# Performance work log

Measured on AMD Instinct MI355X. Metric: run time of the kernel, lower is better.

## Reference

```python
import jax, jax.numpy as jnp
import numpy as np

H = 512

def setup_inputs() -> dict:
    key = jax.random.key(0)
    k1, k2, k3, k4 = jax.random.split(key, 4)
    B, S_dec, S_enc = 8, 2048, 2048
    encoder_output = jax.random.normal(k1, (B, S_enc, H), dtype=jnp.float32)
    decoder_output = jax.random.normal(k2, (B, S_dec, H), dtype=jnp.float32)
    # nn.Bilinear(H, H, 1): weight [1, H, H], bias [1]; init U(-1/sqrt(H), 1/sqrt(H))
    bound = 1.0 / np.sqrt(H)
    W = jax.random.uniform(k3, (1, H, H), dtype=jnp.float32, minval=-bound, maxval=bound)
    b = jax.random.uniform(k4, (1,), dtype=jnp.float32, minval=-bound, maxval=bound)
    return {"encoder_output": encoder_output, "decoder_output": decoder_output, "W": W, "b": b}

def reference(encoder_output, decoder_output, W, b):
    # Original: scores[b,d,e] = Bilinear(enc[b,e], dec[b,d]) = enc[b,e] @ W[0] @ dec[b,d] + bias
    # Computed as two GEMMs instead of expanding to [B, S_dec, S_enc, H].
    encW = jnp.einsum('beh,hg->beg', encoder_output, W[0])   # [B, S_enc, H]
    scores = jnp.einsum('beg,bdg->bde', encW, decoder_output) + b[0]  # [B, S_dec, S_enc]
    return scores
```

## Files before the change

kernel.cpp:

```cpp
#include <hip/hip_runtime.h>

typedef __attribute__((ext_vector_type(8))) short short8;
typedef __attribute__((ext_vector_type(4))) float f32x4;
typedef __attribute__((ext_vector_type(8))) unsigned short ushort8;

__device__ __forceinline__ unsigned short f2bf(float x) {
  union { float f; unsigned u; } v; v.f = x;
  unsigned r = v.u + 0x7fffu + ((v.u >> 16) & 1u);
  return (unsigned short)(r >> 16);
}

__global__ __launch_bounds__(256) void wt_kernel(
    const float* __restrict__ W, unsigned short* __restrict__ Wt) {
  __shared__ float s[64][65];
  int g0 = blockIdx.x * 64, h0 = blockIdx.y * 64;
  int tx = threadIdx.x & 63, ty = threadIdx.x >> 6;
#pragma unroll
  for (int rr = 0; rr < 16; ++rr) {
    int h = ty * 16 + rr;
    s[h][tx] = W[(long)(h0 + h) * 512 + g0 + tx];
  }
  __syncthreads();
#pragma unroll
  for (int rr = 0; rr < 16; ++rr) {
    int g = ty * 16 + rr;
    Wt[(long)(g0 + g) * 512 + h0 + tx] = f2bf(s[tx][g]);
  }
}

__global__ __launch_bounds__(256) void gemm1_plus_cvtdec(
    const float* __restrict__ enc, const unsigned short* __restrict__ Wt,
    unsigned short* __restrict__ encW,
    const float* __restrict__ dec, unsigned short* __restrict__ dec_bf) {
  if (blockIdx.x >= 512) {
    int i = (blockIdx.x - 512) * 256 + threadIdx.x;
    const float4* p = (const float4*)(dec + (long)i * 8);
    float4 a = p[0], b = p[1];
    ushort8 o;
    o[0] = f2bf(a.x); o[1] = f2bf(a.y); o[2] = f2bf(a.z); o[3] = f2bf(a.w);
    o[4] = f2bf(b.x); o[5] = f2bf(b.y); o[6] = f2bf(b.z); o[7] = f2bf(b.w);
    *(ushort8*)(dec_bf + (long)i * 8) = o;
    return;
  }

  constexpr int K = 512, N = 512, BK = 32;
  __shared__ __align__(16) short As[128 * BK];
  __shared__ __align__(16) short Bs[128 * BK];

  const int g = blockIdx.x;
  const int work = (g & 7) * 64 + (g >> 3);
  const int bxm = work >> 2, byn = work & 3;

  const int tid = threadIdx.x;
  const int wave = tid >> 6, lane = tid & 63;
  const int wm = wave >> 1, wn = wave & 1;
  const int r = lane & 15, q = lane >> 4;

  const float* Ab = enc + (long)bxm * 128 * K;
  const unsigned short* Bb = Wt + (long)byn * 128 * K;

  const int srow = tid >> 1, shalf = tid & 1;
  const float* arow = Ab + (long)srow * K + shalf * 16;

  f32x4 acc[4][4] = {};
  float4 av[4];
#pragma unroll
  for (int j = 0; j < 4; ++j) av[j] = ((const float4*)arow)[j];

  for (int kt = 0; kt < K; kt += BK) {
    ushort8 o0, o1;
    o0[0] = f2bf(av[0].x); o0[1] = f2bf(av[0].y); o0[2] = f2bf(av[0].z); o0[3] = f2bf(av[0].w);
    o0[4] = f2bf(av[1].x); o0[5] = f2bf(av[1].y); o0[6] = f2bf(av[1].z); o0[7] = f2bf(av[1].w);
    o1[0] = f2bf(av[2].x); o1[1] = f2bf(av[2].y); o1[2] = f2bf(av[2].z); o1[3] = f2bf(av[2].w);
    o1[4] = f2bf(av[3].x); o1[5] = f2bf(av[3].y); o1[6] = f2bf(av[3].z); o1[7] = f2bf(av[3].w);
    *(ushort8*)&As[srow * BK + shalf * 16 + 0] = o0;
    *(ushort8*)&As[srow * BK + shalf * 16 + 8] = o1;

#pragma unroll
    for (int j = 0; j < 2; ++j) {
      int c = (j * 4 + wave) * 64 + lane;
      int row = c >> 2;
      int coff = (c & 3) * 8;
      __builtin_amdgcn_global_load_lds(
          (const __attribute__((address_space(1))) void*)(Bb + (long)row * K + kt + coff),
          (__attribute__((address_space(3))) void*)(Bs + (j * 4 + wave) * 512),
          16, 0, 0);
    }
    __syncthreads();

    short8 af[4], bfr[4];
#pragma unroll
    for (int m = 0; m < 4; ++m)
      af[m] = *(const short8*)&As[(wm * 64 + m * 16 + r) * BK + q * 8];
#pragma unroll
    for (int n = 0; n < 4; ++n)
      bfr[n] = *(const short8*)&Bs[(wn * 64 + n * 16 + r) * BK + q * 8];

    if (kt + BK < K) {
      const float* ap = arow + kt + BK;
#pragma unroll
      for (int j = 0; j < 4; ++j) av[j] = ((const float4*)ap)[j];
    }

#pragma unroll
    for (int m = 0; m < 4; ++m)
#pragma unroll
      for (int n = 0; n < 4; ++n)
        acc[m][n] = __builtin_amdgcn_mfma_f32_16x16x32_bf16(af[m], bfr[n], acc[m][n], 0, 0, 0);
    __syncthreads();
  }

  const long rowbase = (long)bxm * 128 + wm * 64;
  const long colbase = (long)byn * 128 + wn * 64;
#pragma unroll
  for (int m = 0; m < 4; ++m)
#pragma unroll
    for (int n = 0; n < 4; ++n)
#pragma unroll
      for (int j = 0; j < 4; ++j) {
        long row = rowbase + m * 16 + q * 4 + j;
        long col = colbase + n * 16 + r;
        encW[row * (long)N + col] = f2bf(acc[m][n][j]);
      }
}

#define VMCNT(n) asm volatile("s_waitcnt vmcnt(" #n ")" ::: "memory")
#define LGKM0  asm volatile("s_waitcnt lgkmcnt(0)" ::: "memory")
#define BAR __builtin_amdgcn_s_barrier()

#define LA(p, h) (Lds + (p) * 32768 + (h) * 16384)
#define LB(p, h) (Lds + 65536 + (p) * 32768 + (h) * 16384)

#define STGH(GP, LBASE, T, H)                                                 \
  do {                                                                        \
    _Pragma("unroll") for (int j_ = 0; j_ < 2; ++j_) {                        \
      int c_ = w * 2 + j_;                                                    \
      __builtin_amdgcn_global_load_lds(                                       \
          (const __attribute__((address_space(1))) void*)(                    \
              (GP) + ((long)((H) * 128 + (c_ >> 1) * 16 + srow)) * 512 +      \
              (T) * 64 + (c_ & 1) * 32 + scol),                               \
          (__attribute__((address_space(3))) void*)((LBASE) + (c_ << 10)),    \
          16, 0, 0);                                                          \
    }                                                                         \
  } while (0)

#define LOADAF(p, mh)                                                         \
  _Pragma("unroll") for (int mi_ = 0; mi_ < 4; ++mi_)                         \
    _Pragma("unroll") for (int ks_ = 0; ks_ < 2; ++ks_)                       \
      af[mi_][ks_] = *(const short8*)(LA(p, wm) +                             \
          ((((mh) * 4 + mi_) * 2 + ks_) << 10) + lconst)

#define LOADBF(p, nh)                                                         \
  _Pragma("unroll") for (int n_ = 0; n_ < 2; ++n_)                            \
    _Pragma("unroll") for (int ks_ = 0; ks_ < 2; ++ks_)                       \
      bf[nh][n_][ks_] = *(const short8*)(LB(p, wn >> 1) +                     \
          ((((wn & 1) * 4 + (nh) * 2 + n_) * 2 + ks_) << 10) + lconst)

#define QMFMA(mh, nh)                                                         \
  do {                                                                        \
    BAR;                                                                      \
    LGKM0;                                                                    \
    __builtin_amdgcn_sched_barrier(0);                                        \
    __builtin_amdgcn_s_setprio(1);                                            \
    _Pragma("unroll") for (int mi_ = 0; mi_ < 4; ++mi_)                       \
      _Pragma("unroll") for (int n_ = 0; n_ < 2; ++n_)                        \
        _Pragma("unroll") for (int ks_ = 0; ks_ < 2; ++ks_)                   \
          acc[(mh) * 4 + mi_][(nh) * 2 + n_] =                                \
              __builtin_amdgcn_mfma_f32_16x16x32_bf16(                        \
                  af[mi_][ks_], bf[nh][n_][ks_],                              \
                  acc[(mh) * 4 + mi_][(nh) * 2 + n_], 0, 0, 0);               \
    __builtin_amdgcn_s_setprio(0);                                            \
  } while (0)

__global__ __launch_bounds__(512) void gemm2_8ph2(
    const unsigned short* __restrict__ A,
    const unsigned short* __restrict__ Bt,
    float* __restrict__ C, const float* __restrict__ bias) {
  __shared__ __align__(16) char Lds[131072];

  const int flat = blockIdx.x;
  const int z = flat & 7;
  const int work = flat >> 3;
  const int by = work & 7, bx = work >> 3;

  const int tid = threadIdx.x;
  const int w = tid >> 6, lane = tid & 63;
  const int wm = w >> 2, wn = w & 3;
  const int base_r = lane & 15, q = lane >> 4;
  const int lconst = base_r * 64 + ((q * 16) ^ ((base_r & 8) << 2));
  const int srow = lane >> 2;
  const int scol = ((lane & 3) * 8) ^ (((lane >> 5) & 1) << 4);

  const unsigned short* Ab = A + ((long)z * 2048 + bx * 256) * 512;
  const unsigned short* Bb = Bt + ((long)z * 2048 + by * 256) * 512;

  f32x4 acc[8][4] = {};
  short8 af[4][2];
  short8 bf[2][2][2];

  STGH(Bb, LB(0, 0), 0, 0);
  STGH(Bb, LB(0, 1), 0, 1);
  STGH(Ab, LA(0, 0), 0, 0);
  STGH(Ab, LA(0, 1), 0, 1);
  STGH(Bb, LB(1, 0), 1, 0);
  STGH(Ab, LA(1, 0), 1, 0);
  VMCNT(4);
  BAR;

  for (int t = 0; t < 3; ++t) {
    const int T1v = 2 * t + 1, T2v = 2 * t + 2, T3v = 2 * t + 3;
    LOADAF(0, 0); LOADBF(0, 0);
    STGH(Ab, LA(1, 1), T1v, 1);
    QMFMA(0, 0); BAR;
    LOADBF(0, 1);
    STGH(Bb, LB(1, 1), T1v, 1);
    QMFMA(0, 1); BAR;
    LOADAF(0, 1);
    STGH(Bb, LB(0, 0), T2v, 0);
    QMFMA(1, 0); BAR;
    STGH(Bb, LB(0, 1), T2v, 1);
    QMFMA(1, 1); VMCNT(4); BAR;
    LOADAF(1, 0); LOADBF(1, 0);
    STGH(Ab, LA(0, 0), T2v, 0);
    QMFMA(0, 0); BAR;
    LOADBF(1, 1);
    STGH(Ab, LA(0, 1), T2v, 1);
    QMFMA(0, 1); BAR;
    LOADAF(1, 1);
    STGH(Bb, LB(1, 0), T3v, 0);
    QMFMA(1, 0); BAR;
    STGH(Ab, LA(1, 0), T3v, 0);
    QMFMA(1, 1); VMCNT(4); BAR;
  }
  LOADAF(0, 0); LOADBF(0, 0);
  STGH(Ab, LA(1, 1), 7, 1);
  QMFMA(0, 0); BAR;
  LOADBF(0, 1);
  STGH(Bb, LB(1, 1), 7, 1);
  QMFMA(0, 1); BAR;
  LOADAF(0, 1);               QMFMA(1, 0); BAR;
                              QMFMA(1, 1); VMCNT(0); BAR;
  LOADAF(1, 0); LOADBF(1, 0); QMFMA(0, 0); BAR;
  LOADBF(1, 1);               QMFMA(0, 1); BAR;
  LOADAF(1, 1);               QMFMA(1, 0); BAR;
                              QMFMA(1, 1);

  const float bv = bias[0];
  float* Cb = C + ((long)z * 2048 + bx * 256 + wm * 128) * 2048 + by * 256 + wn * 64;
#pragma unroll
  for (int m = 0; m < 8; ++m)
#pragma unroll
    for (int n = 0; n < 4; ++n)
#pragma unroll
      for (int j = 0; j < 4; ++j)
        Cb[(long)(m * 16 + q * 4 + j) * 2048 + n * 16 + base_r] = acc[m][n][j] + bv;
}

extern "C" void kernel_launch(void* const* d_in, const int* in_sizes, int n_in,
                              void* d_out, int out_size, void* d_ws, size_t ws_size,
                              hipStream_t stream) {
  const float* enc  = (const float*)d_in[0];
  const float* dec  = (const float*)d_in[1];
  const float* W    = (const float*)d_in[2];
  const float* bias = (const float*)d_in[3];
  float* out = (float*)d_out;

  constexpr int Bn = 8, S = 2048, H = 512;
  constexpr long NE = (long)Bn * S * H;

  unsigned short* dec_bf = (unsigned short*)d_ws;
  unsigned short* Wt     = dec_bf + NE;
  unsigned short* encW   = Wt + (long)H * H;

  wt_kernel<<<dim3(8, 8), 256, 0, stream>>>(W, Wt);

  gemm1_plus_cvtdec<<<dim3(512 + 4096, 1, 1), 256, 0, stream>>>(
      enc, Wt, encW, dec, dec_bf);

  gemm2_8ph2<<<dim3(512, 1, 1), 512, 0, stream>>>(dec_bf, encW, out, bias);
}
```

Baseline: 79.57 us.

## Compute two adjacent output tiles per block in second GEMM, reusing A tile

Each block of the second GEMM now computes two horizontally adjacent 256x256 output tiles. It runs one continuous 16-step K pipeline: steps 0-7 use the first B tile and steps 8-15 the second, with the A panel re-streamed each half. The first tile's results are written out mid-loop and the accumulators reset. The grid is halved to 256 blocks, which reduces launch and prologue/epilogue pipeline overhead but may leave compute units idle (256 CUs on MI355X) and serialises the mid-loop store inside the pipeline.

```diff
diff --git a/kernel.cpp b/kernel.cpp
--- a/kernel.cpp
+++ b/kernel.cpp
@@ -138,7 +138,7 @@
       __builtin_amdgcn_global_load_lds(                                       \
           (const __attribute__((address_space(1))) void*)(                    \
               (GP) + ((long)((H) * 128 + (c_ >> 1) * 16 + srow)) * 512 +      \
-              (T) * 64 + (c_ & 1) * 32 + scol),                               \
+              ((T) & 7) * 64 + (c_ & 1) * 32 + scol),                         \
           (__attribute__((address_space(3))) void*)((LBASE) + (c_ << 10)),    \
           16, 0, 0);                                                          \
     }                                                                         \
@@ -172,7 +172,21 @@
     __builtin_amdgcn_s_setprio(0);                                            \
   } while (0)
 
-__global__ __launch_bounds__(512) void gemm2_8ph2(
+#define EPI(BYI)                                                              \
+  do {                                                                        \
+    float* Cb_ = C + ((long)z * 2048 + bx * 256 + wm * 128) * 2048 +          \
+                 (BYI) * 256 + wn * 64;                                       \
+    _Pragma("unroll") for (int m_ = 0; m_ < 8; ++m_)                          \
+      _Pragma("unroll") for (int n_ = 0; n_ < 4; ++n_)                        \
+        _Pragma("unroll") for (int j_ = 0; j_ < 4; ++j_)                      \
+          Cb_[(long)(m_ * 16 + q * 4 + j_) * 2048 + n_ * 16 + base_r] =       \
+              acc[m_][n_][j_] + bv;                                           \
+    _Pragma("unroll") for (int m_ = 0; m_ < 8; ++m_)                          \
+      _Pragma("unroll") for (int n_ = 0; n_ < 4; ++n_)                        \
+        acc[m_][n_] = (f32x4){0.f, 0.f, 0.f, 0.f};                            \
+  } while (0)
+
+__global__ __launch_bounds__(512) void gemm2_2t(
     const unsigned short* __restrict__ A,
     const unsigned short* __restrict__ Bt,
     float* __restrict__ C, const float* __restrict__ bias) {
@@ -181,7 +195,7 @@
   const int flat = blockIdx.x;
   const int z = flat & 7;
   const int work = flat >> 3;
-  const int by = work & 7, bx = work >> 3;
+  const int by2 = work & 3, bx = work >> 2;
 
   const int tid = threadIdx.x;
   const int w = tid >> 6, lane = tid & 63;
@@ -192,33 +206,38 @@
   const int scol = ((lane & 3) * 8) ^ (((lane >> 5) & 1) << 4);
 
   const unsigned short* Ab = A + ((long)z * 2048 + bx * 256) * 512;
-  const unsigned short* Bb = Bt + ((long)z * 2048 + by * 256) * 512;
+  const unsigned short* Bb0 = Bt + ((long)z * 2048 + (by2 * 2) * 256) * 512;
+  const unsigned short* Bb1 = Bb0 + (long)256 * 512;
+  const float bv = bias[0];
 
   f32x4 acc[8][4] = {};
   short8 af[4][2];
   short8 bf[2][2][2];
 
-  STGH(Bb, LB(0, 0), 0, 0);
-  STGH(Bb, LB(0, 1), 0, 1);
+  STGH(Bb0, LB(0, 0), 0, 0);
+  STGH(Bb0, LB(0, 1), 0, 1);
   STGH(Ab, LA(0, 0), 0, 0);
   STGH(Ab, LA(0, 1), 0, 1);
-  STGH(Bb, LB(1, 0), 1, 0);
+  STGH(Bb0, LB(1, 0), 1, 0);
   STGH(Ab, LA(1, 0), 1, 0);
   VMCNT(4);
   BAR;
 
-  for (int t = 0; t < 3; ++t) {
+  for (int t = 0; t < 7; ++t) {
     const int T1v = 2 * t + 1, T2v = 2 * t + 2, T3v = 2 * t + 3;
+    const unsigned short* B1 = (T1v >= 8) ? Bb1 : Bb0;
+    const unsigned short* B2 = (T2v >= 8) ? Bb1 : Bb0;
+    const unsigned short* B3 = (T3v >= 8) ? Bb1 : Bb0;
     LOADAF(0, 0); LOADBF(0, 0);
     STGH(Ab, LA(1, 1), T1v, 1);
     QMFMA(0, 0); BAR;
     LOADBF(0, 1);
-    STGH(Bb, LB(1, 1), T1v, 1);
+    STGH(B1, LB(1, 1), T1v, 1);
     QMFMA(0, 1); BAR;
     LOADAF(0, 1);
-    STGH(Bb, LB(0, 0), T2v, 0);
+    STGH(B2, LB(0, 0), T2v, 0);
     QMFMA(1, 0); BAR;
-    STGH(Bb, LB(0, 1), T2v, 1);
+    STGH(B2, LB(0, 1), T2v, 1);
     QMFMA(1, 1); VMCNT(4); BAR;
     LOADAF(1, 0); LOADBF(1, 0);
     STGH(Ab, LA(0, 0), T2v, 0);
@@ -227,16 +246,17 @@
     STGH(Ab, LA(0, 1), T2v, 1);
     QMFMA(0, 1); BAR;
     LOADAF(1, 1);
-    STGH(Bb, LB(1, 0), T3v, 0);
+    STGH(B3, LB(1, 0), T3v, 0);
     QMFMA(1, 0); BAR;
     STGH(Ab, LA(1, 0), T3v, 0);
     QMFMA(1, 1); VMCNT(4); BAR;
+    if (t == 3) EPI(by2 * 2);
   }
   LOADAF(0, 0); LOADBF(0, 0);
-  STGH(Ab, LA(1, 1), 7, 1);
+  STGH(Ab, LA(1, 1), 15, 1);
   QMFMA(0, 0); BAR;
   LOADBF(0, 1);
-  STGH(Bb, LB(1, 1), 7, 1);
+  STGH(Bb1, LB(1, 1), 15, 1);
   QMFMA(0, 1); BAR;
   LOADAF(0, 1);               QMFMA(1, 0); BAR;
                               QMFMA(1, 1); VMCNT(0); BAR;
@@ -244,16 +264,7 @@
   LOADBF(1, 1);               QMFMA(0, 1); BAR;
   LOADAF(1, 1);               QMFMA(1, 0); BAR;
                               QMFMA(1, 1);
-
-  const float bv = bias[0];
-  float* Cb = C + ((long)z * 2048 + bx * 256 + wm * 128) * 2048 + by * 256 + wn * 64;
-#pragma unroll
-  for (int m = 0; m < 8; ++m)
-#pragma unroll
-    for (int n = 0; n < 4; ++n)
-#pragma unroll
-      for (int j = 0; j < 4; ++j)
-        Cb[(long)(m * 16 + q * 4 + j) * 2048 + n * 16 + base_r] = acc[m][n][j] + bv;
+  EPI(by2 * 2 + 1);
 }
 
 extern "C" void kernel_launch(void* const* d_in, const int* in_sizes, int n_in,
@@ -277,5 +288,5 @@
   gemm1_plus_cvtdec<<<dim3(512 + 4096, 1, 1), 256, 0, stream>>>(
       enc, Wt, encW, dec, dec_bf);
 
-  gemm2_8ph2<<<dim3(512, 1, 1), 512, 0, stream>>>(dec_bf, encW, out, bias);
-}
+  gemm2_2t<<<dim3(256, 1, 1), 512, 0, stream>>>(dec_bf, encW, out, bias);
+}
```

New measurement: 281.9 us. 254% more time.
